# Optimization experiments

Measured on AMD Instinct MI355X. Metric: run time of the kernel, lower is better.

## Reference

```python
import jax, jax.numpy as jnp
import numpy as np

D_MODEL = 1024
NUM_HEADS = 16
MAX_LEN = 2048
HEAD_DIM = D_MODEL // NUM_HEADS
BATCH = 4
SEQ = 1024


def setup_inputs() -> dict:
    key = jax.random.key(0)
    ks = jax.random.split(key, 5)
    return {
        "query": jax.random.normal(ks[0], (BATCH, SEQ, D_MODEL), dtype=jnp.float32),
        "key": jax.random.normal(ks[1], (BATCH, SEQ, D_MODEL), dtype=jnp.float32),
        "value": jax.random.normal(ks[2], (BATCH, SEQ, D_MODEL), dtype=jnp.float32),
        "rel_k": jax.random.normal(ks[3], (MAX_LEN, HEAD_DIM), dtype=jnp.float32),
        "rel_v": jax.random.normal(ks[4], (MAX_LEN, HEAD_DIM), dtype=jnp.float32),
    }


def reference(query, key, value, rel_k, rel_v):
    B, S, D = query.shape
    H, hd = NUM_HEADS, D // NUM_HEADS
    # (B, H, S, hd)
    q = query.reshape(B, S, H, hd).transpose(0, 2, 1, 3)
    k = key.reshape(B, S, H, hd).transpose(0, 2, 1, 3)
    v = value.reshape(B, S, H, hd).transpose(0, 2, 1, 3)
    scale = 1.0 / np.sqrt(hd).astype(np.float32)
    # content scores + relative-position key bias (q . rel_k)
    scores = jnp.einsum("bhqd,bhkd->bhqk", q, k) * scale
    scores = scores + jnp.einsum("bhqd,kd->bhqk", q, rel_k[:S])
    attn = jax.nn.softmax(scores, axis=-1)  # (B, H, S, S)
    out = jnp.einsum("bhqk,bhkd->bhqd", attn, v)
    out = out + jnp.einsum("bhqk,kd->bhqd", attn, rel_v[:S])
    return out.transpose(0, 2, 1, 3).reshape(B, S, D)
```

## Files before the change

kernel.cpp:

```cpp
#include <hip/hip_runtime.h>

#define SQ 1024
#define DM 1024
#define HD 64
#define NBH 64

typedef __attribute__((ext_vector_type(8))) _Float16 v8h;
typedef __attribute__((ext_vector_type(4))) float v4f;
typedef __attribute__((ext_vector_type(2))) __fp16 v2fp16;
typedef __attribute__((ext_vector_type(4))) unsigned int v4u;

__device__ __forceinline__ v4f mfma_f16(v8h a, v8h b, v4f c) {
  return __builtin_amdgcn_mfma_f32_16x16x32_f16(a, b, c, 0, 0, 0);
}

__global__ __launch_bounds__(256) void prep_kernel(
    const float* __restrict__ q, const float* __restrict__ k, const float* __restrict__ v,
    const float* __restrict__ relk, const float* __restrict__ relv,
    _Float16* __restrict__ Qh, _Float16* __restrict__ Kh,
    _Float16* __restrict__ Vth)
{
  __shared__ float vt[64][65];
  int blk = blockIdx.x;
  int st = blk & 15;
  int bh = blk >> 4;
  int b = bh >> 4, h = bh & 15;
  int s0 = st * 64;
  int t = (int)threadIdx.x;
  int d = t & 63, sl4 = t >> 6;
  const float scale = 0.125f;

  #pragma unroll
  for (int i = 0; i < 16; ++i) {
    int sl = sl4 + i * 4;
    int s = s0 + sl;
    size_t gidx = ((size_t)(b * SQ + s)) * DM + h * HD + d;
    float qv = q[gidx];
    float kv = k[gidx] * scale + relk[s * HD + d];
    float vv = v[gidx] + relv[s * HD + d];
    size_t widx = ((size_t)(bh * SQ + s)) * HD + d;
    Qh[widx] = (_Float16)qv;
    Kh[widx] = (_Float16)kv;
    vt[sl][d] = vv;
  }
  __syncthreads();
  int sl = t & 63, d4 = t >> 6;
  #pragma unroll
  for (int i = 0; i < 16; ++i) {
    int dd = d4 + i * 4;
    Vth[((size_t)(bh * HD + dd)) * SQ + s0 + sl] = (_Float16)vt[sl][dd];
  }
}

__global__ __launch_bounds__(256) void attn_kernel(
    const _Float16* __restrict__ Qh, const _Float16* __restrict__ Kh,
    const _Float16* __restrict__ Vth, float* __restrict__ out)
{
  __shared__ v8h KlG[64 * 8];
  __shared__ v8h VlG[64 * 8];

  int tid = (int)threadIdx.x;
  int lane = tid & 63, w = tid >> 6;
  int g = lane >> 4, r15 = lane & 15;
  int bid = (int)blockIdx.x;
  int wk = (bid & 7) * 64 + (bid >> 3);
  int bh = wk >> 3, qt = wk & 7;
  int b = bh >> 4, h = bh & 15;
  int q0 = qt * 128 + w * 32;

  v8h aq[2][2];
  #pragma unroll
  for (int t = 0; t < 2; ++t) {
    const _Float16* qb = Qh + ((size_t)(bh * SQ + q0 + 16 * t + r15)) * HD;
    aq[t][0] = *(const v8h*)(qb + g * 8);
    aq[t][1] = *(const v8h*)(qb + 32 + g * 8);
  }

  const _Float16* kb = Kh + (size_t)bh * SQ * HD;
  const _Float16* vb = Vth + (size_t)bh * HD * SQ;

  v4f o[2][4];
  #pragma unroll
  for (int t = 0; t < 2; ++t)
    #pragma unroll
    for (int c = 0; c < 4; ++c) o[t][c] = (v4f){0.f, 0.f, 0.f, 0.f};
  float m[2] = {-3.0e38f, -3.0e38f}, l[2] = {0.f, 0.f};

  int krow[4];
  #pragma unroll
  for (int c = 0; c < 4; ++c)
    krow[c] = ((c >> 1) << 5) + ((r15 >> 2) << 3) + ((c & 1) << 2) + (r15 & 3);
  int fk = (r15 & 3) | (((r15 >> 2) & 1) << 2);
  int fv = (r15 & 3) | (((r15 >> 3) & 1) << 2);

  for (int t0 = 0; t0 < SQ / 64; ++t0) {
    int k0 = t0 * 64;
    if (t0) __syncthreads();
    #pragma unroll
    for (int i = 0; i < 2; ++i) {
      int seg = tid + i * 256;
      int row = seg >> 3, gr = seg & 7;
      int fs = (row & 3) | (((row >> 3) & 1) << 2);
      v8h kd = *(const v8h*)(kb + ((size_t)(k0 + row)) * HD + gr * 8);
      v8h vd = *(const v8h*)(vb + ((size_t)row) * SQ + k0 + gr * 8);
      KlG[row * 8 + (gr ^ fs)] = kd;
      VlG[row * 8 + (gr ^ fs)] = vd;
    }
    __syncthreads();

    v4f s[2][4];
    #pragma unroll
    for (int c = 0; c < 4; ++c) {
      v8h kf0 = KlG[krow[c] * 8 + (g ^ fk)];
      v8h kf1 = KlG[krow[c] * 8 + ((4 | g) ^ fk)];
      v4f z0 = (v4f){0.f, 0.f, 0.f, 0.f};
      v4f z1 = (v4f){0.f, 0.f, 0.f, 0.f};
      z0 = mfma_f16(kf0, aq[0][0], z0);
      z0 = mfma_f16(kf1, aq[0][1], z0);
      z1 = mfma_f16(kf0, aq[1][0], z1);
      z1 = mfma_f16(kf1, aq[1][1], z1);
      s[0][c] = z0;
      s[1][c] = z1;
    }

    #pragma unroll
    for (int t = 0; t < 2; ++t) {
      float pm = s[t][0][0];
      #pragma unroll
      for (int c = 0; c < 4; ++c)
        #pragma unroll
        for (int r = 0; r < 4; ++r)
          pm = fmaxf(pm, s[t][c][r]);
      if (!__all(pm - m[t] <= 8.f)) {
        pm = fmaxf(pm, __shfl_xor(pm, 16));
        pm = fmaxf(pm, __shfl_xor(pm, 32));
        float mnew = fmaxf(m[t], pm);
        float sc = __expf(m[t] - mnew);
        m[t] = mnew;
        l[t] *= sc;
        #pragma unroll
        for (int c = 0; c < 4; ++c) o[t][c] *= sc;
      }
      float rs = 0.f;
      #pragma unroll
      for (int c = 0; c < 4; ++c)
        #pragma unroll
        for (int r = 0; r < 4; ++r) {
          float p = __expf(s[t][c][r] - m[t]);
          s[t][c][r] = p;
          rs += p;
        }
      l[t] += rs;
    }

    v8h pb0[2], pb1[2];
    #pragma unroll
    for (int t = 0; t < 2; ++t) {
      v4u w0, w1;
      w0[0] = __builtin_bit_cast(unsigned int, __builtin_amdgcn_cvt_pkrtz(s[t][0][0], s[t][0][1]));
      w0[1] = __builtin_bit_cast(unsigned int, __builtin_amdgcn_cvt_pkrtz(s[t][0][2], s[t][0][3]));
      w0[2] = __builtin_bit_cast(unsigned int, __builtin_amdgcn_cvt_pkrtz(s[t][1][0], s[t][1][1]));
      w0[3] = __builtin_bit_cast(unsigned int, __builtin_amdgcn_cvt_pkrtz(s[t][1][2], s[t][1][3]));
      w1[0] = __builtin_bit_cast(unsigned int, __builtin_amdgcn_cvt_pkrtz(s[t][2][0], s[t][2][1]));
      w1[1] = __builtin_bit_cast(unsigned int, __builtin_amdgcn_cvt_pkrtz(s[t][2][2], s[t][2][3]));
      w1[2] = __builtin_bit_cast(unsigned int, __builtin_amdgcn_cvt_pkrtz(s[t][3][0], s[t][3][1]));
      w1[3] = __builtin_bit_cast(unsigned int, __builtin_amdgcn_cvt_pkrtz(s[t][3][2], s[t][3][3]));
      pb0[t] = __builtin_bit_cast(v8h, w0);
      pb1[t] = __builtin_bit_cast(v8h, w1);
    }

    #pragma unroll
    for (int c = 0; c < 4; ++c) {
      int rv = 16 * c + r15;
      v8h vf0 = VlG[rv * 8 + (g ^ fv)];
      v8h vf1 = VlG[rv * 8 + ((4 | g) ^ fv)];
      #pragma unroll
      for (int t = 0; t < 2; ++t) {
        o[t][c] = mfma_f16(vf0, pb0[t], o[t][c]);
        o[t][c] = mfma_f16(vf1, pb1[t], o[t][c]);
      }
    }
  }

  #pragma unroll
  for (int t = 0; t < 2; ++t) {
    float lr = l[t];
    lr += __shfl_xor(lr, 16);
    lr += __shfl_xor(lr, 32);
    float inv = 1.f / lr;
    int qrow = q0 + 16 * t + r15;
    #pragma unroll
    for (int c = 0; c < 4; ++c) {
      v4f res = o[t][c] * inv;
      *(v4f*)(&out[((size_t)(b * SQ + qrow)) * DM + h * HD + 16 * c + 4 * g]) = res;
    }
  }
}

extern "C" void kernel_launch(void* const* d_in, const int* in_sizes, int n_in,
                              void* d_out, int out_size, void* d_ws, size_t ws_size,
                              hipStream_t stream) {
  const float* q = (const float*)d_in[0];
  const float* k = (const float*)d_in[1];
  const float* v = (const float*)d_in[2];
  const float* relk = (const float*)d_in[3];
  const float* relv = (const float*)d_in[4];

  _Float16* Qh = (_Float16*)d_ws;
  _Float16* Kh = Qh + (size_t)NBH * SQ * HD;
  _Float16* Vth = Kh + (size_t)NBH * SQ * HD;

  prep_kernel<<<dim3(NBH * (SQ / 64)), dim3(256), 0, stream>>>(q, k, v, relk, relv, Qh, Kh, Vth);
  attn_kernel<<<dim3(512), dim3(256), 0, stream>>>(Qh, Kh, Vth, (float*)d_out);
}
```

Before: 50.16 us.

## Double-buffer K/V tiles via direct global-to-LDS loads in attention kernel

Replaces the register-staged K/V tile loads with `global_load_lds` 16-byte direct-to-LDS transfers into two LDS buffers. The next tile is prefetched while the current one is used for the QK and PV MFMAs, which leaves one barrier per iteration instead of two. The XOR swizzle moves from the LDS write address to the global source address so that each lane's LDS destination is contiguous. This doubles LDS use and depends on the compiler inserting the right vmcnt waits before the barrier.

```diff
diff --git a/kernel.cpp b/kernel.cpp
--- a/kernel.cpp
+++ b/kernel.cpp
@@ -10,8 +10,15 @@
 typedef __attribute__((ext_vector_type(2))) __fp16 v2fp16;
 typedef __attribute__((ext_vector_type(4))) unsigned int v4u;
 
+typedef __attribute__((address_space(3))) void as3_void;
+typedef __attribute__((address_space(1))) const void as1_cvoid;
+
 __device__ __forceinline__ v4f mfma_f16(v8h a, v8h b, v4f c) {
   return __builtin_amdgcn_mfma_f32_16x16x32_f16(a, b, c, 0, 0, 0);
+}
+
+__device__ __forceinline__ void gload16(const _Float16* g, v8h* l) {
+  __builtin_amdgcn_global_load_lds((as1_cvoid*)g, (as3_void*)l, 16, 0, 0);
 }
 
 __global__ __launch_bounds__(256) void prep_kernel(
@@ -56,8 +63,8 @@
     const _Float16* __restrict__ Qh, const _Float16* __restrict__ Kh,
     const _Float16* __restrict__ Vth, float* __restrict__ out)
 {
-  __shared__ v8h KlG[64 * 8];
-  __shared__ v8h VlG[64 * 8];
+  __shared__ v8h KlG[2][512];
+  __shared__ v8h VlG[2][512];
 
   int tid = (int)threadIdx.x;
   int lane = tid & 63, w = tid >> 6;
@@ -79,6 +86,19 @@
   const _Float16* kb = Kh + (size_t)bh * SQ * HD;
   const _Float16* vb = Vth + (size_t)bh * HD * SQ;
 
+  size_t kOff[2], vOff[2];
+  int ldsG[2];
+  #pragma unroll
+  for (int j = 0; j < 2; ++j) {
+    int G = w * 128 + j * 64 + lane;
+    int row = G >> 3, gr = G & 7;
+    int fs = (row & 3) | (((row >> 3) & 1) << 2);
+    int src = gr ^ fs;
+    kOff[j] = (size_t)row * HD + src * 8;
+    vOff[j] = (size_t)row * SQ + src * 8;
+    ldsG[j] = w * 128 + j * 64;
+  }
+
   v4f o[2][4];
   #pragma unroll
   for (int t = 0; t < 2; ++t)
@@ -93,26 +113,30 @@
   int fk = (r15 & 3) | (((r15 >> 2) & 1) << 2);
   int fv = (r15 & 3) | (((r15 >> 3) & 1) << 2);
 
+  #pragma unroll
+  for (int j = 0; j < 2; ++j) {
+    gload16(kb + kOff[j], &KlG[0][ldsG[j]]);
+    gload16(vb + vOff[j], &VlG[0][ldsG[j]]);
+  }
+  __syncthreads();
+
   for (int t0 = 0; t0 < SQ / 64; ++t0) {
-    int k0 = t0 * 64;
-    if (t0) __syncthreads();
-    #pragma unroll
-    for (int i = 0; i < 2; ++i) {
-      int seg = tid + i * 256;
-      int row = seg >> 3, gr = seg & 7;
-      int fs = (row & 3) | (((row >> 3) & 1) << 2);
-      v8h kd = *(const v8h*)(kb + ((size_t)(k0 + row)) * HD + gr * 8);
-      v8h vd = *(const v8h*)(vb + ((size_t)row) * SQ + k0 + gr * 8);
-      KlG[row * 8 + (gr ^ fs)] = kd;
-      VlG[row * 8 + (gr ^ fs)] = vd;
-    }
-    __syncthreads();
+    int cur = t0 & 1;
+    if (t0 < SQ / 64 - 1) {
+      size_t kT = (size_t)(t0 + 1) * 64 * HD;
+      size_t vT = (size_t)(t0 + 1) * 64;
+      #pragma unroll
+      for (int j = 0; j < 2; ++j) {
+        gload16(kb + kT + kOff[j], &KlG[cur ^ 1][ldsG[j]]);
+        gload16(vb + vT + vOff[j], &VlG[cur ^ 1][ldsG[j]]);
+      }
+    }
 
     v4f s[2][4];
     #pragma unroll
     for (int c = 0; c < 4; ++c) {
-      v8h kf0 = KlG[krow[c] * 8 + (g ^ fk)];
-      v8h kf1 = KlG[krow[c] * 8 + ((4 | g) ^ fk)];
+      v8h kf0 = KlG[cur][krow[c] * 8 + (g ^ fk)];
+      v8h kf1 = KlG[cur][krow[c] * 8 + ((4 | g) ^ fk)];
       v4f z0 = (v4f){0.f, 0.f, 0.f, 0.f};
       v4f z1 = (v4f){0.f, 0.f, 0.f, 0.f};
       z0 = mfma_f16(kf0, aq[0][0], z0);
@@ -172,14 +196,16 @@
     #pragma unroll
     for (int c = 0; c < 4; ++c) {
       int rv = 16 * c + r15;
-      v8h vf0 = VlG[rv * 8 + (g ^ fv)];
-      v8h vf1 = VlG[rv * 8 + ((4 | g) ^ fv)];
+      v8h vf0 = VlG[cur][rv * 8 + (g ^ fv)];
+      v8h vf1 = VlG[cur][rv * 8 + ((4 | g) ^ fv)];
       #pragma unroll
       for (int t = 0; t < 2; ++t) {
         o[t][c] = mfma_f16(vf0, pb0[t], o[t][c]);
         o[t][c] = mfma_f16(vf1, pb1[t], o[t][c]);
       }
     }
+
+    __syncthreads();
   }
 
   #pragma unroll
```

New measurement: 50.42 us. No clear change (+0.5%).
